# Kernel optimization log

Measured on AMD Instinct MI355X. Metric: run time of the kernel, lower is better.

## Reference

```python
import jax, jax.numpy as jnp
import numpy as np

N_NODES = 50000
N_EDGES = 800000
IN_DIM = 128
HID = 32
HEADS = 4
OUT_DIM = 2
NEG_SLOPE = 0.2


def gat_conv(feat, W, al, ar, bias, src, dst, n_nodes):
    """DGL GATConv (eval mode, no dropout). feat: [N, Fin]; W: [Fin, H*D];
    al, ar: [H, D]; bias: [H*D]. Returns [N, H, D]."""
    H, D = al.shape
    hf = (feat @ W).reshape(n_nodes, H, D)              # [N,H,D]
    el = jnp.einsum('nhd,hd->nh', hf, al)               # [N,H]
    er = jnp.einsum('nhd,hd->nh', hf, ar)               # [N,H]
    e = el[src] + er[dst]                               # [E,H]
    e = jax.nn.leaky_relu(e, NEG_SLOPE)
    # segment softmax over incoming edges of each dst node
    emax = jax.ops.segment_max(e, dst, num_segments=n_nodes)  # [N,H]
    emax = jnp.where(jnp.isfinite(emax), emax, 0.0)
    ex = jnp.exp(e - emax[dst])                         # [E,H]
    denom = jax.ops.segment_sum(ex, dst, num_segments=n_nodes)  # [N,H]
    alpha = ex / jnp.maximum(denom[dst], 1e-30)         # [E,H]
    msg = hf[src] * alpha[:, :, None]                   # [E,H,D]
    out = jax.ops.segment_sum(msg, dst, num_segments=n_nodes)   # [N,H,D]
    return out + bias.reshape(1, H, D)


def setup_inputs() -> dict:
    key = jax.random.key(0)
    ks = jax.random.split(key, 16)
    f32 = jnp.float32
    in_feat = jax.random.normal(ks[0], (N_NODES, IN_DIM), dtype=f32)
    src = jax.random.randint(ks[1], (N_EDGES,), 0, N_NODES)
    dst = jax.random.randint(ks[2], (N_EDGES,), 0, N_NODES)
    s1 = 1.0 / np.sqrt(IN_DIM)
    s2 = 1.0 / np.sqrt(HID * HEADS)
    W1 = jax.random.normal(ks[3], (IN_DIM, HEADS * HID), dtype=f32) * s1
    al1 = jax.random.normal(ks[4], (HEADS, HID), dtype=f32) * 0.1
    ar1 = jax.random.normal(ks[5], (HEADS, HID), dtype=f32) * 0.1
    b1 = jnp.zeros((HEADS * HID,), dtype=f32)
    W2 = jax.random.normal(ks[6], (HEADS * HID, HEADS * HID), dtype=f32) * s2
    al2 = jax.random.normal(ks[7], (HEADS, HID), dtype=f32) * 0.1
    ar2 = jax.random.normal(ks[8], (HEADS, HID), dtype=f32) * 0.1
    b2 = jnp.zeros((HEADS * HID,), dtype=f32)
    Wout = jax.random.normal(ks[9], (HID, OUT_DIM), dtype=f32) * (1.0 / np.sqrt(HID))
    bout = jnp.zeros((OUT_DIM,), dtype=f32)
    return {"in_feat": in_feat, "W1": W1, "al1": al1, "ar1": ar1, "b1": b1,
            "W2": W2, "al2": al2, "ar2": ar2, "b2": b2,
            "Wout": Wout, "bout": bout, "src": src, "dst": dst}


def reference(in_feat, W1, al1, ar1, b1, W2, al2, ar2, b2, Wout, bout, src, dst):
    h = gat_conv(in_feat, W1, al1, ar1, b1, src, dst, N_NODES)  # [N,H,D]
    h = jax.nn.relu(h.reshape(N_NODES, HEADS * HID))            # flatten(1) + relu
    h = gat_conv(h, W2, al2, ar2, b2, src, dst, N_NODES)        # [N,H,D]
    emd = h.mean(axis=1)                                        # mean over heads -> [N,D]
    logits = jax.nn.relu(emd) @ Wout + bout                     # [N,2]
    return jax.nn.softmax(logits, axis=-1)
```

## Files before the change

kernel.cpp:

```cpp
#include <hip/hip_runtime.h>
#include <cmath>

#define N_NODES 50000
#define N_EDGES 800000
#define NBUCK 196
#define NHB 196
#define EPB 4096

typedef unsigned short u16;
typedef unsigned int u32;
typedef __attribute__((ext_vector_type(8))) short bf16x8;
typedef __attribute__((ext_vector_type(4))) float f32x4;

static __device__ __forceinline__ float lrelu(float x) { return x > 0.f ? x : 0.2f * x; }
static __device__ __forceinline__ float bf2f(u16 u) { return __uint_as_float(((u32)u) << 16); }
static __device__ __forceinline__ float bflo(u32 u) { return __uint_as_float(u << 16); }
static __device__ __forceinline__ float bfhi(u32 u) { return __uint_as_float(u & 0xFFFF0000u); }
static __device__ __forceinline__ u16 f2bf(float f) {
    u32 b = __float_as_uint(f);
    return (u16)((b + 0x7FFFu + ((b >> 16) & 1u)) >> 16);
}
static __device__ __forceinline__ u32 pack2(float a, float b) {
    return (u32)f2bf(a) | ((u32)f2bf(b) << 16);
}

__global__ __launch_bounds__(1024) void bhist_k(const int* __restrict__ dst, u32* __restrict__ bcnt) {
    __shared__ u32 hist[NBUCK];
    int tid = threadIdx.x;
    for (int i = tid; i < NBUCK; i += 1024) hist[i] = 0;
    __syncthreads();
    int base = blockIdx.x * EPB;
#pragma unroll
    for (int k = 0; k < 4; ++k) {
        int e = base + k * 1024 + tid;
        if (e < N_EDGES) atomicAdd(&hist[dst[e] >> 8], 1u);
    }
    __syncthreads();
    for (int i = tid; i < NBUCK; i += 1024) bcnt[(size_t)blockIdx.x * NBUCK + i] = hist[i];
}

__global__ __launch_bounds__(256) void bscan_k(const u32* __restrict__ bcnt, u32* __restrict__ wbase,
                                               int* __restrict__ bstart) {
    __shared__ int s[256];
    int t = threadIdx.x;
    u32 run = 0;
    if (t < NBUCK) {
        for (int blk = 0; blk < NHB; ++blk) {
            u32 v = bcnt[(size_t)blk * NBUCK + t];
            wbase[(size_t)blk * NBUCK + t] = run;
            run += v;
        }
    }
    s[t] = (t < NBUCK) ? (int)run : 0;
    __syncthreads();
    for (int o = 1; o < 256; o <<= 1) {
        int v = (t >= o) ? s[t - o] : 0;
        __syncthreads();
        s[t] += v;
        __syncthreads();
    }
    if (t < NBUCK) bstart[t] = (t == 0) ? 0 : s[t - 1];
    if (t == NBUCK - 1) bstart[NBUCK] = s[t];
}

__global__ __launch_bounds__(1024) void bscatter_k(const int* __restrict__ src, const int* __restrict__ dst,
                                                   const u32* __restrict__ wbase, const int* __restrict__ bstart,
                                                   u32* __restrict__ bucketed) {
    __shared__ u32 pos[NBUCK];
    int tid = threadIdx.x;
    for (int i = tid; i < NBUCK; i += 1024)
        pos[i] = (u32)bstart[i] + wbase[(size_t)blockIdx.x * NBUCK + i];
    __syncthreads();
    int base = blockIdx.x * EPB;
#pragma unroll
    for (int k = 0; k < 4; ++k) {
        int e = base + k * 1024 + tid;
        if (e < N_EDGES) {
            int d = dst[e];
            int b = d >> 8;
            u32 p = atomicAdd(&pos[b], 1u);
            bucketed[p] = (u32)src[e] | ((u32)(d & 255) << 16);
        }
    }
}

__global__ __launch_bounds__(256) void bcsr_k(const u32* __restrict__ bucketed, const int* __restrict__ bstart,
                                              int* __restrict__ offs, u16* __restrict__ srcs) {
    __shared__ u32 cnt[256];
    __shared__ int s[256];
    __shared__ u32 fp[256];
    int b = blockIdx.x;
    int tid = threadIdx.x;
    int ebeg = bstart[b], eend = bstart[b + 1];
    int ne = eend - ebeg;
    cnt[tid] = 0;
    __syncthreads();
    for (int i = tid; i < ne; i += 256)
        atomicAdd(&cnt[bucketed[ebeg + i] >> 16], 1u);
    __syncthreads();
    s[tid] = (int)cnt[tid];
    __syncthreads();
    for (int o = 1; o < 256; o <<= 1) {
        int v = (tid >= o) ? s[tid - o] : 0;
        __syncthreads();
        s[tid] += v;
        __syncthreads();
    }
    int excl = s[tid] - (int)cnt[tid];
    int node = b * 256 + tid;
    if (node < N_NODES) offs[node] = ebeg + excl;
    if (b == NBUCK - 1 && tid == 0) offs[N_NODES] = N_EDGES;
    fp[tid] = (u32)excl;
    __syncthreads();
    for (int i = tid; i < ne; i += 256) {
        u32 u = bucketed[ebeg + i];
        u32 p = atomicAdd(&fp[u >> 16], 1u);
        srcs[ebeg + p] = (u16)(u & 0xFFFFu);
    }
}

__global__ __launch_bounds__(256) void packW_k(const float* __restrict__ W, u16* __restrict__ Wp) {
    int i = blockIdx.x * 256 + threadIdx.x;
    if (i >= 16384) return;
    int j = i & 7, lane = (i >> 3) & 63, ks = (i >> 9) & 3, nt = i >> 11;
    int k = ks * 32 + (lane >> 4) * 8 + j;
    int ncol = nt * 16 + (lane & 15);
    Wp[i] = f2bf(W[k * 128 + ncol]);
}

template <int BF16IN>
__global__ __launch_bounds__(256) void gemm_mfma(
    const void* __restrict__ Xv, const u16* __restrict__ Wp,
    const float* __restrict__ al, const float* __restrict__ ar,
    u16* __restrict__ hf, float* __restrict__ el, float* __restrict__ er, int n)
{
    __shared__ u16 xs[64][136];
    int row0 = blockIdx.x * 64;
    int tid = threadIdx.x;
    if (BF16IN) {
        const uint4* Xb = (const uint4*)Xv;
        for (int i = tid; i < 1024; i += 256) {
            int r = i >> 4, c = i & 15;
            uint4 v = make_uint4(0u, 0u, 0u, 0u);
            if (row0 + r < n) v = Xb[(size_t)(row0 + r) * 16 + c];
            ((uint4*)&xs[r][0])[c] = v;
        }
    } else {
        const float4* X4 = (const float4*)Xv;
        for (int i = tid; i < 2048; i += 256) {
            int r = i >> 5, c = i & 31;
            float4 v = make_float4(0.f, 0.f, 0.f, 0.f);
            if (row0 + r < n) v = X4[(size_t)(row0 + r) * 32 + c];
            ((uint2*)&xs[r][0])[c] = make_uint2(pack2(v.x, v.y), pack2(v.z, v.w));
        }
    }
    __syncthreads();

    int wave = tid >> 6, lane = tid & 63;
    int quad = lane >> 4, l15 = lane & 15;

    bf16x8 bfrag[2][4];
#pragma unroll
    for (int ct = 0; ct < 2; ++ct) {
        int nt = wave * 2 + ct;
#pragma unroll
        for (int ks = 0; ks < 4; ++ks)
            bfrag[ct][ks] = *(const bf16x8*)(Wp + ((((nt * 4 + ks) * 64) + lane) << 3));
    }

    f32x4 acc[4][2];
#pragma unroll
    for (int rt = 0; rt < 4; ++rt)
#pragma unroll
        for (int ct = 0; ct < 2; ++ct)
            acc[rt][ct] = (f32x4){0.f, 0.f, 0.f, 0.f};

#pragma unroll
    for (int ks = 0; ks < 4; ++ks) {
#pragma unroll
        for (int rt = 0; rt < 4; ++rt) {
            bf16x8 a = *(const bf16x8*)&xs[rt * 16 + l15][ks * 32 + quad * 8];
            acc[rt][0] = __builtin_amdgcn_mfma_f32_16x16x32_bf16(a, bfrag[0][ks], acc[rt][0], 0, 0, 0);
            acc[rt][1] = __builtin_amdgcn_mfma_f32_16x16x32_bf16(a, bfrag[1][ks], acc[rt][1], 0, 0, 0);
        }
    }

    float alv0 = al[wave * 32 + l15], alv1 = al[wave * 32 + 16 + l15];
    float arv0 = ar[wave * 32 + l15], arv1 = ar[wave * 32 + 16 + l15];
#pragma unroll
    for (int rt = 0; rt < 4; ++rt) {
#pragma unroll
        for (int r = 0; r < 4; ++r) {
            int row = row0 + rt * 16 + quad * 4 + r;
            float c0 = acc[rt][0][r], c1 = acc[rt][1][r];
            if (row < n) {
                hf[(size_t)row * 128 + wave * 32 + l15] = f2bf(c0);
                hf[(size_t)row * 128 + wave * 32 + 16 + l15] = f2bf(c1);
            }
            float pel = c0 * alv0 + c1 * alv1;
            float per = c0 * arv0 + c1 * arv1;
            pel += __shfl_xor(pel, 1); pel += __shfl_xor(pel, 2);
            pel += __shfl_xor(pel, 4); pel += __shfl_xor(pel, 8);
            per += __shfl_xor(per, 1); per += __shfl_xor(per, 2);
            per += __shfl_xor(per, 4); per += __shfl_xor(per, 8);
            if (l15 == 0 && row < n) {
                el[row * 4 + wave] = pel;
                er[row * 4 + wave] = per;
            }
        }
    }
}

static __device__ __forceinline__ void agg_core(
    int node, int lane, const int* __restrict__ offs, const u16* __restrict__ srcs,
    const float* __restrict__ el, const float* __restrict__ er, const u16* __restrict__ hf,
    float acc[8], float& den)
{
    int qw = lane >> 4;
    int q = lane & 15;
    int h = q >> 2;
    float erh = er[node * 4 + h];
    int beg = offs[node], end = offs[node + 1];
    den = 0.f;
#pragma unroll
    for (int i = 0; i < 8; i++) acc[i] = 0.f;
    int base = beg;
    for (; base + 8 <= end; base += 8) {
        int s0 = srcs[base + qw];
        int s1 = srcs[base + 4 + qw];
        float w0 = __expf(lrelu(el[s0 * 4 + h] + erh));
        float w1 = __expf(lrelu(el[s1 * 4 + h] + erh));
        uint4 u0 = *(const uint4*)(hf + (size_t)s0 * 128 + q * 8);
        uint4 u1 = *(const uint4*)(hf + (size_t)s1 * 128 + q * 8);
        den += w0 + w1;
        acc[0] += w0 * bflo(u0.x) + w1 * bflo(u1.x);
        acc[1] += w0 * bfhi(u0.x) + w1 * bfhi(u1.x);
        acc[2] += w0 * bflo(u0.y) + w1 * bflo(u1.y);
        acc[3] += w0 * bfhi(u0.y) + w1 * bfhi(u1.y);
        acc[4] += w0 * bflo(u0.z) + w1 * bflo(u1.z);
        acc[5] += w0 * bfhi(u0.z) + w1 * bfhi(u1.z);
        acc[6] += w0 * bflo(u0.w) + w1 * bflo(u1.w);
        acc[7] += w0 * bfhi(u0.w) + w1 * bfhi(u1.w);
    }
    for (; base < end; base += 4) {
        int e = base + qw;
        bool valid = e < end;
        int ec = valid ? e : end - 1;
        int s = srcs[ec];
        float w = valid ? __expf(lrelu(el[s * 4 + h] + erh)) : 0.f;
        uint4 u = *(const uint4*)(hf + (size_t)s * 128 + q * 8);
        den += w;
        acc[0] += w * bflo(u.x);
        acc[1] += w * bfhi(u.x);
        acc[2] += w * bflo(u.y);
        acc[3] += w * bfhi(u.y);
        acc[4] += w * bflo(u.z);
        acc[5] += w * bfhi(u.z);
        acc[6] += w * bflo(u.w);
        acc[7] += w * bfhi(u.w);
    }
#pragma unroll
    for (int i = 0; i < 8; i++) {
        acc[i] += __shfl_xor(acc[i], 16);
        acc[i] += __shfl_xor(acc[i], 32);
    }
    den += __shfl_xor(den, 16);
    den += __shfl_xor(den, 32);
}

__global__ __launch_bounds__(256) void agg1_k(const int* __restrict__ offs, const u16* __restrict__ srcs,
                                              const float* __restrict__ el, const float* __restrict__ er,
                                              const u16* __restrict__ hf, const float* __restrict__ bias,
                                              u16* __restrict__ h1) {
    int node = blockIdx.x * 4 + (threadIdx.x >> 6);
    int lane = threadIdx.x & 63;
    if (node >= N_NODES) return;
    float acc[8], den;
    agg_core(node, lane, offs, srcs, el, er, hf, acc, den);
    int qw = lane >> 4, q = lane & 15;
    if (qw == 0) {
        float inv = 1.0f / fmaxf(den, 1e-30f);
        float o[8];
#pragma unroll
        for (int i = 0; i < 8; i++)
            o[i] = fmaxf(acc[i] * inv + bias[q * 8 + i], 0.f);
        uint4 pk;
        pk.x = pack2(o[0], o[1]);
        pk.y = pack2(o[2], o[3]);
        pk.z = pack2(o[4], o[5]);
        pk.w = pack2(o[6], o[7]);
        *(uint4*)(h1 + (size_t)node * 128 + q * 8) = pk;
    }
}

__global__ __launch_bounds__(256) void agg2_k(const int* __restrict__ offs, const u16* __restrict__ srcs,
                                              const float* __restrict__ el, const float* __restrict__ er,
                                              const u16* __restrict__ hf, const float* __restrict__ bias,
                                              const float* __restrict__ Wout, const float* __restrict__ bout,
                                              float2* __restrict__ out) {
    int node = blockIdx.x * 4 + (threadIdx.x >> 6);
    int lane = threadIdx.x & 63;
    if (node >= N_NODES) return;
    float acc[8], den;
    agg_core(node, lane, offs, srcs, el, er, hf, acc, den);
    int q = lane & 15;
    float inv = 1.0f / fmaxf(den, 1e-30f);
    float o[8];
#pragma unroll
    for (int i = 0; i < 8; i++) o[i] = acc[i] * inv + bias[q * 8 + i];
#pragma unroll
    for (int i = 0; i < 8; i++) {
        o[i] += __shfl_xor(o[i], 4);
        o[i] += __shfl_xor(o[i], 8);
        o[i] = fmaxf(0.25f * o[i], 0.f);
    }
    int d0 = (q & 3) * 8;
    float l0 = 0.f, l1 = 0.f;
#pragma unroll
    for (int i = 0; i < 8; i++) {
        l0 += o[i] * Wout[(d0 + i) * 2];
        l1 += o[i] * Wout[(d0 + i) * 2 + 1];
    }
    l0 += __shfl_xor(l0, 1); l0 += __shfl_xor(l0, 2);
    l1 += __shfl_xor(l1, 1); l1 += __shfl_xor(l1, 2);
    if (lane == 0) {
        l0 += bout[0];
        l1 += bout[1];
        float mx = fmaxf(l0, l1);
        float e0 = __expf(l0 - mx), e1 = __expf(l1 - mx);
        float invs = 1.f / (e0 + e1);
        out[node] = make_float2(e0 * invs, e1 * invs);
    }
}

extern "C" void kernel_launch(void* const* d_in, const int* in_sizes, int n_in,
                              void* d_out, int out_size, void* d_ws, size_t ws_size,
                              hipStream_t stream) {
    const float* in_feat = (const float*)d_in[0];
    const float* W1   = (const float*)d_in[1];
    const float* al1  = (const float*)d_in[2];
    const float* ar1  = (const float*)d_in[3];
    const float* b1   = (const float*)d_in[4];
    const float* W2   = (const float*)d_in[5];
    const float* al2  = (const float*)d_in[6];
    const float* ar2  = (const float*)d_in[7];
    const float* b2   = (const float*)d_in[8];
    const float* Wout = (const float*)d_in[9];
    const float* bout = (const float*)d_in[10];
    const int*   src  = (const int*)d_in[11];
    const int*   dst  = (const int*)d_in[12];
    float* out = (float*)d_out;

    char* ws = (char*)d_ws;
    size_t off = 0;
    auto carve = [&](size_t bytes) {
        char* p = ws + off;
        off = (off + bytes + 255) & ~(size_t)255;
        return p;
    };
    u16*   hfA      = (u16*)carve((size_t)N_NODES * 128 * 2);
    u16*   h1       = (u16*)carve((size_t)N_NODES * 128 * 2);
    float* el       = (float*)carve((size_t)N_NODES * 4 * 4);
    float* er       = (float*)carve((size_t)N_NODES * 4 * 4);
    u16*   srcs     = (u16*)carve((size_t)N_EDGES * 2);
    u32*   bucketed = (u32*)carve((size_t)N_EDGES * 4);
    u32*   bcnt     = (u32*)carve((size_t)NHB * NBUCK * 4);
    u32*   wbase    = (u32*)carve((size_t)NHB * NBUCK * 4);
    int*   bstart   = (int*)carve((size_t)(NBUCK + 1) * 4);
    int*   offs     = (int*)carve((size_t)(N_NODES + 1) * 4);
    u16*   Wp1      = (u16*)carve((size_t)16384 * 2);
    u16*   Wp2      = (u16*)carve((size_t)16384 * 2);
    (void)ws_size; (void)in_sizes; (void)n_in; (void)out_size;

    const int GB = (N_NODES + 63) / 64;
    const int AB = (N_NODES + 3) / 4;

    bhist_k<<<NHB, 1024, 0, stream>>>(dst, bcnt);
    packW_k<<<64, 256, 0, stream>>>(W1, Wp1);
    packW_k<<<64, 256, 0, stream>>>(W2, Wp2);
    bscan_k<<<1, 256, 0, stream>>>(bcnt, wbase, bstart);
    bscatter_k<<<NHB, 1024, 0, stream>>>(src, dst, wbase, bstart, bucketed);
    bcsr_k<<<NBUCK, 256, 0, stream>>>(bucketed, bstart, offs, srcs);

    gemm_mfma<0><<<GB, 256, 0, stream>>>(in_feat, Wp1, al1, ar1, hfA, el, er, N_NODES);
    agg1_k<<<AB, 256, 0, stream>>>(offs, srcs, el, er, hfA, b1, h1);

    gemm_mfma<1><<<GB, 256, 0, stream>>>(h1, Wp2, al2, ar2, hfA, el, er, N_NODES);
    agg2_k<<<AB, 256, 0, stream>>>(offs, srcs, el, er, hfA, b2, Wout, bout, (float2*)out);
}
```

Before: 226.3 us.

## Quantize node features to int8 per head, parallelize bucket scan, stage sources in registers

Stores projected node features as int8 with a per-row, per-head scale instead of bf16. This halves the bytes gathered per edge in both aggregation passes. The aggregation loop now loads up to 64 source indices into lanes once per node and shuffles them out, and unrolls by 16 edges to get more loads in flight. The single-block serial bucket scan becomes a transposed per-bucket parallel scan plus a small second scan, and the two weight-pack launches are merged into one. The int8 quantization lowers feature precision, which risks accuracy against the tolerance.

```diff
diff --git a/kernel.cpp b/kernel.cpp
--- a/kernel.cpp
+++ b/kernel.cpp
@@ -14,14 +14,15 @@
 
 static __device__ __forceinline__ float lrelu(float x) { return x > 0.f ? x : 0.2f * x; }
 static __device__ __forceinline__ float bf2f(u16 u) { return __uint_as_float(((u32)u) << 16); }
-static __device__ __forceinline__ float bflo(u32 u) { return __uint_as_float(u << 16); }
-static __device__ __forceinline__ float bfhi(u32 u) { return __uint_as_float(u & 0xFFFF0000u); }
 static __device__ __forceinline__ u16 f2bf(float f) {
     u32 b = __float_as_uint(f);
     return (u16)((b + 0x7FFFu + ((b >> 16) & 1u)) >> 16);
 }
 static __device__ __forceinline__ u32 pack2(float a, float b) {
     return (u32)f2bf(a) | ((u32)f2bf(b) << 16);
+}
+static __device__ __forceinline__ float sx(u32 u, int k) {
+    return (float)((int)(u << ((3 - k) * 8)) >> 24);
 }
 
 __global__ __launch_bounds__(1024) void bhist_k(const int* __restrict__ dst, u32* __restrict__ bcnt) {
@@ -36,31 +37,40 @@
         if (e < N_EDGES) atomicAdd(&hist[dst[e] >> 8], 1u);
     }
     __syncthreads();
-    for (int i = tid; i < NBUCK; i += 1024) bcnt[(size_t)blockIdx.x * NBUCK + i] = hist[i];
-}
-
-__global__ __launch_bounds__(256) void bscan_k(const u32* __restrict__ bcnt, u32* __restrict__ wbase,
-                                               int* __restrict__ bstart) {
-    __shared__ int s[256];
+    for (int i = tid; i < NBUCK; i += 1024) bcnt[(size_t)i * NHB + blockIdx.x] = hist[i];
+}
+
+__global__ __launch_bounds__(256) void scant_k(const u32* __restrict__ bcnt, u32* __restrict__ wbase,
+                                               u32* __restrict__ btot) {
+    __shared__ u32 s[256];
+    int i = blockIdx.x, t = threadIdx.x;
+    u32 v = (t < NHB) ? bcnt[(size_t)i * NHB + t] : 0;
+    s[t] = v;
+    __syncthreads();
+    for (int o = 1; o < 256; o <<= 1) {
+        u32 x = (t >= o) ? s[t - o] : 0;
+        __syncthreads();
+        s[t] += x;
+        __syncthreads();
+    }
+    if (t < NHB) wbase[(size_t)i * NHB + t] = s[t] - v;
+    if (t == 255) btot[i] = s[255];
+}
+
+__global__ __launch_bounds__(256) void scanb2_k(const u32* __restrict__ btot, int* __restrict__ bstart) {
+    __shared__ u32 s[256];
     int t = threadIdx.x;
-    u32 run = 0;
-    if (t < NBUCK) {
-        for (int blk = 0; blk < NHB; ++blk) {
-            u32 v = bcnt[(size_t)blk * NBUCK + t];
-            wbase[(size_t)blk * NBUCK + t] = run;
-            run += v;
-        }
-    }
-    s[t] = (t < NBUCK) ? (int)run : 0;
+    u32 v = (t < NBUCK) ? btot[t] : 0;
+    s[t] = v;
     __syncthreads();
     for (int o = 1; o < 256; o <<= 1) {
-        int v = (t >= o) ? s[t - o] : 0;
-        __syncthreads();
-        s[t] += v;
-        __syncthreads();
-    }
-    if (t < NBUCK) bstart[t] = (t == 0) ? 0 : s[t - 1];
-    if (t == NBUCK - 1) bstart[NBUCK] = s[t];
+        u32 x = (t >= o) ? s[t - o] : 0;
+        __syncthreads();
+        s[t] += x;
+        __syncthreads();
+    }
+    if (t < NBUCK) bstart[t] = (int)(s[t] - v);
+    if (t == NBUCK - 1) bstart[NBUCK] = (int)s[t];
 }
 
 __global__ __launch_bounds__(1024) void bscatter_k(const int* __restrict__ src, const int* __restrict__ dst,
@@ -69,7 +79,7 @@
     __shared__ u32 pos[NBUCK];
     int tid = threadIdx.x;
     for (int i = tid; i < NBUCK; i += 1024)
-        pos[i] = (u32)bstart[i] + wbase[(size_t)blockIdx.x * NBUCK + i];
+        pos[i] = (u32)bstart[i] + wbase[(size_t)i * NHB + blockIdx.x];
     __syncthreads();
     int base = blockIdx.x * EPB;
 #pragma unroll
@@ -119,9 +129,12 @@
     }
 }
 
-__global__ __launch_bounds__(256) void packW_k(const float* __restrict__ W, u16* __restrict__ Wp) {
-    int i = blockIdx.x * 256 + threadIdx.x;
-    if (i >= 16384) return;
+__global__ __launch_bounds__(256) void packW_k(const float* __restrict__ W1, const float* __restrict__ W2,
+                                               u16* __restrict__ Wp1, u16* __restrict__ Wp2) {
+    int gi = blockIdx.x * 256 + threadIdx.x;
+    const float* W = (gi < 16384) ? W1 : W2;
+    u16* Wp = (gi < 16384) ? Wp1 : Wp2;
+    int i = gi & 16383;
     int j = i & 7, lane = (i >> 3) & 63, ks = (i >> 9) & 3, nt = i >> 11;
     int k = ks * 32 + (lane >> 4) * 8 + j;
     int ncol = nt * 16 + (lane & 15);
@@ -132,7 +145,8 @@
 __global__ __launch_bounds__(256) void gemm_mfma(
     const void* __restrict__ Xv, const u16* __restrict__ Wp,
     const float* __restrict__ al, const float* __restrict__ ar,
-    u16* __restrict__ hf, float* __restrict__ el, float* __restrict__ er, int n)
+    signed char* __restrict__ hq, float* __restrict__ hs,
+    float* __restrict__ el, float* __restrict__ er, int n)
 {
     __shared__ u16 xs[64][136];
     int row0 = blockIdx.x * 64;
@@ -193,9 +207,17 @@
         for (int r = 0; r < 4; ++r) {
             int row = row0 + rt * 16 + quad * 4 + r;
             float c0 = acc[rt][0][r], c1 = acc[rt][1][r];
+            float m = fmaxf(fabsf(c0), fabsf(c1));
+            m = fmaxf(m, __shfl_xor(m, 1));
+            m = fmaxf(m, __shfl_xor(m, 2));
+            m = fmaxf(m, __shfl_xor(m, 4));
+            m = fmaxf(m, __shfl_xor(m, 8));
+            m = fmaxf(m, 1e-20f);
+            float qsc = 127.0f / m;
             if (row < n) {
-                hf[(size_t)row * 128 + wave * 32 + l15] = f2bf(c0);
-                hf[(size_t)row * 128 + wave * 32 + 16 + l15] = f2bf(c1);
+                hq[(size_t)row * 128 + wave * 32 + l15] = (signed char)(int)rintf(c0 * qsc);
+                hq[(size_t)row * 128 + wave * 32 + 16 + l15] = (signed char)(int)rintf(c1 * qsc);
+                if (l15 == 0) hs[row * 4 + wave] = m * (1.0f / 127.0f);
             }
             float pel = c0 * alv0 + c1 * alv1;
             float per = c0 * arv0 + c1 * arv1;
@@ -213,7 +235,8 @@
 
 static __device__ __forceinline__ void agg_core(
     int node, int lane, const int* __restrict__ offs, const u16* __restrict__ srcs,
-    const float* __restrict__ el, const float* __restrict__ er, const u16* __restrict__ hf,
+    const float* __restrict__ el, const float* __restrict__ er,
+    const signed char* __restrict__ hq, const float* __restrict__ hs,
     float acc[8], float& den)
 {
     int qw = lane >> 4;
@@ -221,43 +244,102 @@
     int h = q >> 2;
     float erh = er[node * 4 + h];
     int beg = offs[node], end = offs[node + 1];
+    int deg = end - beg;
     den = 0.f;
 #pragma unroll
     for (int i = 0; i < 8; i++) acc[i] = 0.f;
-    int base = beg;
-    for (; base + 8 <= end; base += 8) {
-        int s0 = srcs[base + qw];
-        int s1 = srcs[base + 4 + qw];
-        float w0 = __expf(lrelu(el[s0 * 4 + h] + erh));
-        float w1 = __expf(lrelu(el[s1 * 4 + h] + erh));
-        uint4 u0 = *(const uint4*)(hf + (size_t)s0 * 128 + q * 8);
-        uint4 u1 = *(const uint4*)(hf + (size_t)s1 * 128 + q * 8);
-        den += w0 + w1;
-        acc[0] += w0 * bflo(u0.x) + w1 * bflo(u1.x);
-        acc[1] += w0 * bfhi(u0.x) + w1 * bfhi(u1.x);
-        acc[2] += w0 * bflo(u0.y) + w1 * bflo(u1.y);
-        acc[3] += w0 * bfhi(u0.y) + w1 * bfhi(u1.y);
-        acc[4] += w0 * bflo(u0.z) + w1 * bflo(u1.z);
-        acc[5] += w0 * bfhi(u0.z) + w1 * bfhi(u1.z);
-        acc[6] += w0 * bflo(u0.w) + w1 * bflo(u1.w);
-        acc[7] += w0 * bfhi(u0.w) + w1 * bfhi(u1.w);
-    }
-    for (; base < end; base += 4) {
-        int e = base + qw;
-        bool valid = e < end;
-        int ec = valid ? e : end - 1;
-        int s = srcs[ec];
-        float w = valid ? __expf(lrelu(el[s * 4 + h] + erh)) : 0.f;
-        uint4 u = *(const uint4*)(hf + (size_t)s * 128 + q * 8);
-        den += w;
-        acc[0] += w * bflo(u.x);
-        acc[1] += w * bfhi(u.x);
-        acc[2] += w * bflo(u.y);
-        acc[3] += w * bfhi(u.y);
-        acc[4] += w * bflo(u.z);
-        acc[5] += w * bfhi(u.z);
-        acc[6] += w * bflo(u.w);
-        acc[7] += w * bfhi(u.w);
+
+    if (deg <= 64) {
+        int psrc = (lane < deg) ? (int)srcs[beg + lane] : 0;
+        int base = beg;
+        for (; base + 16 <= end; base += 16) {
+            int j = base - beg + qw;
+            int ss[4];
+            ss[0] = __shfl(psrc, j);
+            ss[1] = __shfl(psrc, j + 4);
+            ss[2] = __shfl(psrc, j + 8);
+            ss[3] = __shfl(psrc, j + 12);
+            float ee[4], sv[4];
+            uint2 uv[4];
+#pragma unroll
+            for (int k = 0; k < 4; ++k) {
+                ee[k] = el[ss[k] * 4 + h];
+                sv[k] = hs[ss[k] * 4 + h];
+                uv[k] = *(const uint2*)(hq + (size_t)ss[k] * 128 + q * 8);
+            }
+#pragma unroll
+            for (int k = 0; k < 4; ++k) {
+                float w = __expf(lrelu(ee[k] + erh));
+                float ws = w * sv[k];
+                den += w;
+                acc[0] += ws * sx(uv[k].x, 0);
+                acc[1] += ws * sx(uv[k].x, 1);
+                acc[2] += ws * sx(uv[k].x, 2);
+                acc[3] += ws * sx(uv[k].x, 3);
+                acc[4] += ws * sx(uv[k].y, 0);
+                acc[5] += ws * sx(uv[k].y, 1);
+                acc[6] += ws * sx(uv[k].y, 2);
+                acc[7] += ws * sx(uv[k].y, 3);
+            }
+        }
+        for (; base + 8 <= end; base += 8) {
+            int j = base - beg + qw;
+            int s0 = __shfl(psrc, j);
+            int s1 = __shfl(psrc, j + 4);
+            float e0 = el[s0 * 4 + h], e1 = el[s1 * 4 + h];
+            float v0 = hs[s0 * 4 + h], v1 = hs[s1 * 4 + h];
+            uint2 u0 = *(const uint2*)(hq + (size_t)s0 * 128 + q * 8);
+            uint2 u1 = *(const uint2*)(hq + (size_t)s1 * 128 + q * 8);
+            float w0 = __expf(lrelu(e0 + erh));
+            float w1 = __expf(lrelu(e1 + erh));
+            float ws0 = w0 * v0, ws1 = w1 * v1;
+            den += w0 + w1;
+            acc[0] += ws0 * sx(u0.x, 0) + ws1 * sx(u1.x, 0);
+            acc[1] += ws0 * sx(u0.x, 1) + ws1 * sx(u1.x, 1);
+            acc[2] += ws0 * sx(u0.x, 2) + ws1 * sx(u1.x, 2);
+            acc[3] += ws0 * sx(u0.x, 3) + ws1 * sx(u1.x, 3);
+            acc[4] += ws0 * sx(u0.y, 0) + ws1 * sx(u1.y, 0);
+            acc[5] += ws0 * sx(u0.y, 1) + ws1 * sx(u1.y, 1);
+            acc[6] += ws0 * sx(u0.y, 2) + ws1 * sx(u1.y, 2);
+            acc[7] += ws0 * sx(u0.y, 3) + ws1 * sx(u1.y, 3);
+        }
+        for (; base < end; base += 4) {
+            int e = base + qw;
+            bool valid = e < end;
+            int j = valid ? (e - beg) : 0;
+            int s = __shfl(psrc, j);
+            float w = valid ? __expf(lrelu(el[s * 4 + h] + erh)) : 0.f;
+            float ws = w * hs[s * 4 + h];
+            uint2 u = *(const uint2*)(hq + (size_t)s * 128 + q * 8);
+            den += w;
+            acc[0] += ws * sx(u.x, 0);
+            acc[1] += ws * sx(u.x, 1);
+            acc[2] += ws * sx(u.x, 2);
+            acc[3] += ws * sx(u.x, 3);
+            acc[4] += ws * sx(u.y, 0);
+            acc[5] += ws * sx(u.y, 1);
+            acc[6] += ws * sx(u.y, 2);
+            acc[7] += ws * sx(u.y, 3);
+        }
+    } else {
+        for (int base = beg; base < end; base += 4) {
+            int e = base + qw;
+            bool valid = e < end;
+            int ec = valid ? e : end - 1;
+            int s = srcs[ec];
+            float w = valid ? __expf(lrelu(el[s * 4 + h] + erh)) : 0.f;
+            float ws = w * hs[s * 4 + h];
+            uint2 u = *(const uint2*)(hq + (size_t)s * 128 + q * 8);
+            den += w;
+            acc[0] += ws * sx(u.x, 0);
+            acc[1] += ws * sx(u.x, 1);
+            acc[2] += ws * sx(u.x, 2);
+            acc[3] += ws * sx(u.x, 3);
+            acc[4] += ws * sx(u.y, 0);
+            acc[5] += ws * sx(u.y, 1);
+            acc[6] += ws * sx(u.y, 2);
+            acc[7] += ws * sx(u.y, 3);
+        }
     }
 #pragma unroll
     for (int i = 0; i < 8; i++) {
@@ -270,13 +352,13 @@
 
 __global__ __launch_bounds__(256) void agg1_k(const int* __restrict__ offs, const u16* __restrict__ srcs,
                                               const float* __restrict__ el, const float* __restrict__ er,
-                                              const u16* __restrict__ hf, const float* __restrict__ bias,
-                                              u16* __restrict__ h1) {
+                                              const signed char* __restrict__ hq, const float* __restrict__ hs,
+                                              const float* __restrict__ bias, u16* __restrict__ h1) {
     int node = blockIdx.x * 4 + (threadIdx.x >> 6);
     int lane = threadIdx.x & 63;
     if (node >= N_NODES) return;
     float acc[8], den;
-    agg_core(node, lane, offs, srcs, el, er, hf, acc, den);
+    agg_core(node, lane, offs, srcs, el, er, hq, hs, acc, den);
     int qw = lane >> 4, q = lane & 15;
     if (qw == 0) {
         float inv = 1.0f / fmaxf(den, 1e-30f);
@@ -295,14 +377,15 @@
 
 __global__ __launch_bounds__(256) void agg2_k(const int* __restrict__ offs, const u16* __restrict__ srcs,
                                               const float* __restrict__ el, const float* __restrict__ er,
-                                              const u16* __restrict__ hf, const float* __restrict__ bias,
+                                              const signed char* __restrict__ hq, const float* __restrict__ hs,
+                                              const float* __restrict__ bias,
                                               const float* __restrict__ Wout, const float* __restrict__ bout,
                                               float2* __restrict__ out) {
     int node = blockIdx.x * 4 + (threadIdx.x >> 6);
     int lane = threadIdx.x & 63;
     if (node >= N_NODES) return;
     float acc[8], den;
-    agg_core(node, lane, offs, srcs, el, er, hf, acc, den);
+    agg_core(node, lane, offs, srcs, el, er, hq, hs, acc, den);
     int q = lane & 15;
     float inv = 1.0f / fmaxf(den, 1e-30f);
     float o[8];
@@ -358,33 +441,35 @@
         off = (off + bytes + 255) & ~(size_t)255;
         return p;
     };
-    u16*   hfA      = (u16*)carve((size_t)N_NODES * 128 * 2);
-    u16*   h1       = (u16*)carve((size_t)N_NODES * 128 * 2);
-    float* el       = (float*)carve((size_t)N_NODES * 4 * 4);
-    float* er       = (float*)carve((size_t)N_NODES * 4 * 4);
-    u16*   srcs     = (u16*)carve((size_t)N_EDGES * 2);
-    u32*   bucketed = (u32*)carve((size_t)N_EDGES * 4);
-    u32*   bcnt     = (u32*)carve((size_t)NHB * NBUCK * 4);
-    u32*   wbase    = (u32*)carve((size_t)NHB * NBUCK * 4);
-    int*   bstart   = (int*)carve((size_t)(NBUCK + 1) * 4);
-    int*   offs     = (int*)carve((size_t)(N_NODES + 1) * 4);
-    u16*   Wp1      = (u16*)carve((size_t)16384 * 2);
-    u16*   Wp2      = (u16*)carve((size_t)16384 * 2);
+    signed char* hq  = (signed char*)carve((size_t)N_NODES * 128);
+    float* hs        = (float*)carve((size_t)N_NODES * 4 * 4);
+    u16*   h1        = (u16*)carve((size_t)N_NODES * 128 * 2);
+    float* el        = (float*)carve((size_t)N_NODES * 4 * 4);
+    float* er        = (float*)carve((size_t)N_NODES * 4 * 4);
+    u16*   srcs      = (u16*)carve((size_t)N_EDGES * 2);
+    u32*   bucketed  = (u32*)carve((size_t)N_EDGES * 4);
+    u32*   bcnt      = (u32*)carve((size_t)NBUCK * NHB * 4);
+    u32*   wbase     = (u32*)carve((size_t)NBUCK * NHB * 4);
+    u32*   btot      = (u32*)carve((size_t)NBUCK * 4);
+    int*   bstart    = (int*)carve((size_t)(NBUCK + 1) * 4);
+    int*   offs      = (int*)carve((size_t)(N_NODES + 1) * 4);
+    u16*   Wp1       = (u16*)carve((size_t)16384 * 2);
+    u16*   Wp2       = (u16*)carve((size_t)16384 * 2);
     (void)ws_size; (void)in_sizes; (void)n_in; (void)out_size;
 
     const int GB = (N_NODES + 63) / 64;
     const int AB = (N_NODES + 3) / 4;
 
     bhist_k<<<NHB, 1024, 0, stream>>>(dst, bcnt);
-    packW_k<<<64, 256, 0, stream>>>(W1, Wp1);
-    packW_k<<<64, 256, 0, stream>>>(W2, Wp2);
-    bscan_k<<<1, 256, 0, stream>>>(bcnt, wbase, bstart);
+    packW_k<<<128, 256, 0, stream>>>(W1, W2, Wp1, Wp2);
+    scant_k<<<NBUCK, 256, 0, stream>>>(bcnt, wbase, btot);
+    scanb2_k<<<1, 256, 0, stream>>>(btot, bstart);
     bscatter_k<<<NHB, 1024, 0, stream>>>(src, dst, wbase, bstart, bucketed);
     bcsr_k<<<NBUCK, 256, 0, stream>>>(bucketed, bstart, offs, srcs);
 
-    gemm_mfma<0><<<GB, 256, 0, stream>>>(in_feat, Wp1, al1, ar1, hfA, el, er, N_NODES);
-    agg1_k<<<AB, 256, 0, stream>>>(offs, srcs, el, er, hfA, b1, h1);
-
-    gemm_mfma<1><<<GB, 256, 0, stream>>>(h1, Wp2, al2, ar2, hfA, el, er, N_NODES);
-    agg2_k<<<AB, 256, 0, stream>>>(offs, srcs, el, er, hfA, b2, Wout, bout, (float2*)out);
-}
+    gemm_mfma<0><<<GB, 256, 0, stream>>>(in_feat, Wp1, al1, ar1, hq, hs, el, er, N_NODES);
+    agg1_k<<<AB, 256, 0, stream>>>(offs, srcs, el, er, hq, hs, b1, h1);
+
+    gemm_mfma<1><<<GB, 256, 0, stream>>>(h1, Wp2, al2, ar2, hq, hs, el, er, N_NODES);
+    agg2_k<<<AB, 256, 0, stream>>>(offs, srcs, el, er, hq, hs, b2, Wout, bout, (float2*)out);
+}
```

Result: faster. 220.6 us (-2.5%).
